# Optimization experiments

Hardware: AMD Instinct MI355X
Metric: run time of the kernel (lower is better)

Reference implementation:

```python
import jax, jax.numpy as jnp
import numpy as np

L, D, H, FF, V = 8, 768, 8, 2048, 32000
MAXLEN, TMAX = 512, 4
S = MAXLEN * TMAX  # 2048 context length
HD = D // H
EPS = 1e-4  # layer_norm_eps from module defaults


def setup_inputs() -> dict:
    key = jax.random.key(0)
    ks = jax.random.split(key, 16)
    s = 0.02
    B = 1
    rn = lambda k, shape: jax.random.normal(k, shape, jnp.float32) * s
    # sinusoidal positional encoding over MAXLEN real-token positions
    pos = np.arange(MAXLEN)[:, None]
    div = np.exp(np.arange(0, D, 2) * (-np.log(10000.0) / D))
    pe = np.zeros((MAXLEN, D), np.float32)
    pe[:, 0::2] = np.sin(pos * div)
    pe[:, 1::2] = np.cos(pos * div)
    return {
        "state_embeddings": jax.random.normal(ks[0], (B, S, D), jnp.float32),
        "padding_mask": jnp.zeros((B, S), bool),
        "pe": jnp.asarray(pe),
        "thought_emb": rn(ks[1], (TMAX, D)),
        "w_qkv": rn(ks[2], (L, 3 * D, D)),
        "b_qkv": jnp.zeros((L, 3 * D), jnp.float32),
        "w_out": rn(ks[3], (L, D, D)),
        "b_out": jnp.zeros((L, D), jnp.float32),
        "ln1_g": jnp.ones((L, D), jnp.float32),
        "ln1_b": jnp.zeros((L, D), jnp.float32),
        "ln2_g": jnp.ones((L, D), jnp.float32),
        "ln2_b": jnp.zeros((L, D), jnp.float32),
        "w_ff1": rn(ks[4], (L, FF, D)),
        "b_ff1": jnp.zeros((L, FF), jnp.float32),
        "w_ff2": rn(ks[5], (L, D, FF)),
        "b_ff2": jnp.zeros((L, D), jnp.float32),
        "fn_g": jnp.ones((D,), jnp.float32),
        "fn_b": jnp.zeros((D,), jnp.float32),
        "w_policy": rn(ks[6], (V, D)),
        "w_v1": rn(ks[7], (FF, D)),
        "b_v1": jnp.zeros((FF,), jnp.float32),
        "w_v2": rn(ks[8], (1, FF)),
        "b_v2": jnp.zeros((1,), jnp.float32),
        "n_thoughts_taken": 3,
    }


def _layer_norm(x, g, b):
    m = x.mean(-1, keepdims=True)
    v = ((x - m) ** 2).mean(-1, keepdims=True)
    return (x - m) / jnp.sqrt(v + EPS) * g + b


def reference(state_embeddings, padding_mask, pe, thought_emb, w_qkv, b_qkv, w_out, b_out, ln1_g, ln1_b, ln2_g, ln2_b, w_ff1, b_ff1, w_ff2, b_ff2, fn_g, fn_b, w_policy, w_v1, b_v1, w_v2, b_v2, n_thoughts_taken):
    tt = int(n_thoughts_taken)
    T = tt + 1  # block size (token + thoughts taken)
    B = state_embeddings.shape[0]
    R = MAXLEN  # real_token_count: all token slots real (no padding)
    # --- DualPositionalEncoding ---
    x = state_embeddings[:, :MAXLEN * T].reshape(B, MAXLEN, T, D)
    x = x + pe[None, :, None, :] + thought_emb[None, None, :T, :]
    x = x.reshape(B, MAXLEN * T, D)
    x = jnp.pad(x, ((0, 0), (0, S - MAXLEN * T), (0, 0)))
    # --- ThoughtsFormer block-causal mask (keep=True means attend) ---
    i = jnp.arange(S)
    tok, off = i // T, i % T
    same_block = (tok[:, None] == tok[None, :]) & (off[:, None] >= off[None, :]) & (tok[:, None] < R)
    global_cols = (off[None, :] == 0) & (tok[None, :] < R) & (i[:, None] > i[None, :]) & (i[:, None] < R * T)
    keep = (same_block | global_cols)[None, None] & (~padding_mask)[:, None, None, :]
    scale = 1.0 / np.sqrt(HD)

    def layer(h, p):
        wq, bq, wo, bo, g1, b1, g2, b2, wf1, bf1, wf2, bf2 = p
        # pre-norm self-attention
        y = _layer_norm(h, g1, b1)
        q, k, v = jnp.split(y @ wq.T + bq, 3, axis=-1)
        q = q.reshape(B, S, H, HD)
        k = k.reshape(B, S, H, HD)
        v = v.reshape(B, S, H, HD)
        scores = jnp.einsum('bihd,bjhd->bhij', q, k) * scale
        attn = jax.nn.softmax(jnp.where(keep, scores, -jnp.inf), axis=-1)
        o = jnp.einsum('bhij,bjhd->bihd', attn, v).reshape(B, S, D)
        h = h + o @ wo.T + bo
        # pre-norm FFN with exact (erf) GELU
        y = _layer_norm(h, g2, b2)
        h = h + jax.nn.gelu(y @ wf1.T + bf1, approximate=False) @ wf2.T + bf2
        h = jnp.where(jnp.isnan(h), 0.0, h)
        return h, None

    x, _ = jax.lax.scan(layer, x, (w_qkv, b_qkv, w_out, b_out, ln1_g, ln1_b, ln2_g, ln2_b, w_ff1, b_ff1, w_ff2, b_ff2))
    x = _layer_norm(x, fn_g, fn_b)  # TransformerEncoder final norm
    logits = x @ w_policy.T  # policy head (no bias)
    values = jax.nn.gelu(x @ w_v1.T + b_v1, approximate=False) @ w_v2.T + b_v2
    return logits, values
```

## Files before the change

### kernel.cpp

```cpp
#include <hip/hip_runtime.h>
#include <math.h>

#define S_TOT 2048
#define DMODEL 768
#define QKVD 2304
#define NHEAD 8
#define HDIM 96
#define FFDIM 2048
#define VOCAB 32000
#define MAXLEN_C 512
#define POL_CHUNK 3200
#define VLT_LD 2080
#define NEG_BIG (-3.0e38f)
#define M_INIT (-1.0e30f)
#define QK_SCALE 0.10206207261596575f

typedef __bf16 bf16x8 __attribute__((ext_vector_type(8)));
typedef float f32x4 __attribute__((ext_vector_type(4)));
typedef unsigned short u16x8 __attribute__((ext_vector_type(8)));
typedef unsigned short u16x4 __attribute__((ext_vector_type(4)));

__device__ __forceinline__ float gelu_exact(float x) {
  return 0.5f * x * (1.0f + erff(x * 0.70710678118654752f));
}

__device__ __forceinline__ float bf2f(unsigned short u) {
  union { unsigned int i; float f; } v;
  v.i = ((unsigned int)u) << 16;
  return v.f;
}

__device__ __forceinline__ unsigned short f2bf(float f) {
  union { float f; unsigned int i; } v;
  v.f = f;
  unsigned int x = v.i;
  return (unsigned short)((x + 0x7fffu + ((x >> 16) & 1u)) >> 16);
}

__device__ __forceinline__ unsigned int pack2bf(float a, float b) {
  return (unsigned int)f2bf(a) | ((unsigned int)f2bf(b) << 16);
}

__device__ __forceinline__ void gload_lds16(const unsigned short* g, unsigned short* l) {
  __builtin_amdgcn_global_load_lds(
      (const __attribute__((address_space(1))) unsigned int*)g,
      (__attribute__((address_space(3))) unsigned int*)l, 16, 0, 0);
}

__global__ __launch_bounds__(256) void embed_kernel(
    const float* __restrict__ se, const float* __restrict__ pe,
    const float* __restrict__ th, const int* __restrict__ ntt,
    float* __restrict__ X) {
  int idx = blockIdx.x * 256 + threadIdx.x;
  if (idx >= S_TOT * DMODEL) return;
  int p = idx / DMODEL;
  int d = idx - p * DMODEL;
  int T = ntt[0] + 1;
  float v = 0.0f;
  if (p < MAXLEN_C * T) {
    v = se[idx] + pe[(p / T) * DMODEL + d] + th[(p % T) * DMODEL + d];
  }
  X[idx] = v;
}

__global__ __launch_bounds__(256) void ln_bf_kernel(
    const float* __restrict__ X, const float* __restrict__ g,
    const float* __restrict__ b, unsigned short* __restrict__ Y) {
  __shared__ float red[4];
  const int row = blockIdx.x;
  const int tid = threadIdx.x;
  const float* x = X + (size_t)row * DMODEL;
  float v0 = x[tid], v1 = x[tid + 256], v2 = x[tid + 512];
  float s = v0 + v1 + v2;
  for (int o = 32; o; o >>= 1) s += __shfl_xor(s, o);
  if ((tid & 63) == 0) red[tid >> 6] = s;
  __syncthreads();
  float mean = (red[0] + red[1] + red[2] + red[3]) * (1.0f / DMODEL);
  float d0 = v0 - mean, d1 = v1 - mean, d2 = v2 - mean;
  float s2 = d0 * d0 + d1 * d1 + d2 * d2;
  for (int o = 32; o; o >>= 1) s2 += __shfl_xor(s2, o);
  __syncthreads();
  if ((tid & 63) == 0) red[tid >> 6] = s2;
  __syncthreads();
  float var = (red[0] + red[1] + red[2] + red[3]) * (1.0f / DMODEL);
  float rstd = rsqrtf(var + 1e-4f);
  unsigned short* y = Y + (size_t)row * DMODEL;
  y[tid]       = f2bf(d0 * rstd * g[tid]       + b[tid]);
  y[tid + 256] = f2bf(d1 * rstd * g[tid + 256] + b[tid + 256]);
  y[tid + 512] = f2bf(d2 * rstd * g[tid + 512] + b[tid + 512]);
}

__global__ __launch_bounds__(256) void cvt_kernel(
    const float* __restrict__ s, unsigned short* __restrict__ d, int n) {
  int i = (blockIdx.x * 256 + threadIdx.x) * 4;
  if (i >= n) return;
  float4 v = *(const float4*)(s + i);
  u16x4 o;
  o[0] = f2bf(v.x); o[1] = f2bf(v.y); o[2] = f2bf(v.z); o[3] = f2bf(v.w);
  *(u16x4*)(d + i) = o;
}

__global__ __launch_bounds__(256) void cvt4_kernel(
    const float* __restrict__ s0, const float* __restrict__ s1,
    const float* __restrict__ s2, const float* __restrict__ s3,
    unsigned short* __restrict__ d0, unsigned short* __restrict__ d1,
    unsigned short* __restrict__ d2, unsigned short* __restrict__ d3,
    int n0, int n1, int n2, int n3) {
  int i = (blockIdx.x * 256 + threadIdx.x) * 4;
  const float* s;
  unsigned short* d;
  if (i < n0) { s = s0; d = d0; }
  else if (i < n0 + n1) { i -= n0; s = s1; d = d1; }
  else if (i < n0 + n1 + n2) { i -= n0 + n1; s = s2; d = d2; }
  else if (i < n0 + n1 + n2 + n3) { i -= n0 + n1 + n2; s = s3; d = d3; }
  else return;
  float4 v = *(const float4*)(s + i);
  u16x4 o;
  o[0] = f2bf(v.x); o[1] = f2bf(v.y); o[2] = f2bf(v.z); o[3] = f2bf(v.w);
  *(u16x4*)(d + i) = o;
}

__global__ __launch_bounds__(256) void cvt6_kernel(
    const float* __restrict__ s0, const float* __restrict__ s1,
    const float* __restrict__ s2, const float* __restrict__ s3,
    const float* __restrict__ s4, const float* __restrict__ s5,
    unsigned short* __restrict__ d0, unsigned short* __restrict__ d1,
    unsigned short* __restrict__ d2, unsigned short* __restrict__ d3,
    unsigned short* __restrict__ d4, unsigned short* __restrict__ d5,
    int n0, int n1, int n2, int n3, int n4, int n5) {
  int i = (blockIdx.x * 256 + threadIdx.x) * 4;
  const float* s;
  unsigned short* d;
  if (i < n0) { s = s0; d = d0; }
  else if (i < n0 + n1) { i -= n0; s = s1; d = d1; }
  else if (i < n0 + n1 + n2) { i -= n0 + n1; s = s2; d = d2; }
  else if (i < n0 + n1 + n2 + n3) { i -= n0 + n1 + n2; s = s3; d = d3; }
  else if (i < n0 + n1 + n2 + n3 + n4) { i -= n0 + n1 + n2 + n3; s = s4; d = d4; }
  else if (i < n0 + n1 + n2 + n3 + n4 + n5) { i -= n0 + n1 + n2 + n3 + n4; s = s5; d = d5; }
  else return;
  float4 v = *(const float4*)(s + i);
  u16x4 o;
  o[0] = f2bf(v.x); o[1] = f2bf(v.y); o[2] = f2bf(v.z); o[3] = f2bf(v.w);
  *(u16x4*)(d + i) = o;
}

__global__ __launch_bounds__(256) void gemm_bf16_kernel(
    const unsigned short* __restrict__ A, const unsigned short* __restrict__ B,
    const float* __restrict__ bias, const float* __restrict__ res,
    void* __restrict__ Cout, int M, int N, int K, int ldc, int act, int outbf,
    int swiz) {
  __shared__ __align__(16) unsigned short As[3 * 4096];
  __shared__ __align__(16) unsigned short Bs[3 * 4096];
  const int t = threadIdx.x;
  const int w = t >> 6, l = t & 63;
  int n_blk, m_blk;
  if (swiz) {
    const int g = blockIdx.x;
    const int chunk = gridDim.x >> 3;
    const int logical = (g & 7) * chunk + (g >> 3);
    m_blk = logical & 15;
    n_blk = logical >> 4;
  } else {
    n_blk = blockIdx.x; m_blk = blockIdx.y;
  }
  const int n0 = n_blk * 128, i0 = m_blk * 128;
  const int wr = w >> 1, wc = w & 1;
  const int lr = l & 15;
  const int koff = (l >> 4) * 8;

  f32x4 acc[4][4] = {};

  const int srow = t >> 2;
  const int scol = (t & 3) * 8;
  const unsigned short* Ag = A + (size_t)(i0 + srow) * K + scol;
  const unsigned short* Bg = B + (size_t)(n0 + srow) * K + scol;
  const int lo0 = (w << 9);
  const int lo1 = 2048 + (w << 9);

#define STAGE128(buf, k0)                                        \
  do {                                                           \
    gload_lds16(Ag + (k0), &As[(buf) * 4096 + lo0]);             \
    gload_lds16(Ag + (size_t)64 * K + (k0), &As[(buf) * 4096 + lo1]); \
    gload_lds16(Bg + (k0), &Bs[(buf) * 4096 + lo0]);             \
    gload_lds16(Bg + (size_t)64 * K + (k0), &Bs[(buf) * 4096 + lo1]); \
  } while (0)

#define COMPUTE128(buf)                                                   \
  do {                                                                    \
    const unsigned short* Ab = &As[(buf) * 4096];                         \
    const unsigned short* Bb = &Bs[(buf) * 4096];                         \
    bf16x8 af[4], bfr[4];                                                 \
    _Pragma("unroll") for (int fi = 0; fi < 4; ++fi)                      \
        af[fi] = *(const bf16x8*)&Ab[(wr * 64 + fi * 16 + lr) * 32 + koff]; \
    _Pragma("unroll") for (int fj = 0; fj < 4; ++fj)                      \
        bfr[fj] = *(const bf16x8*)&Bb[(wc * 64 + fj * 16 + lr) * 32 + koff]; \
    _Pragma("unroll") for (int fi = 0; fi < 4; ++fi)                      \
      _Pragma("unroll") for (int fj = 0; fj < 4; ++fj)                    \
          acc[fi][fj] = __builtin_amdgcn_mfma_f32_16x16x32_bf16(          \
              bfr[fj], af[fi], acc[fi][fj], 0, 0, 0);                     \
  } while (0)

  const int nt = K >> 5;
  STAGE128(0, 0);
  if (nt > 1) STAGE128(1, 32);
  for (int tt = 0; tt < nt; ++tt) {
    const int cb = tt % 3;
    if (tt + 2 < nt) {
      STAGE128((tt + 2) % 3, (tt + 2) << 5);
      asm volatile("s_waitcnt vmcnt(8)" ::: "memory");
    } else if (tt + 1 < nt) {
      asm volatile("s_waitcnt vmcnt(4)" ::: "memory");
    } else {
      asm volatile("s_waitcnt vmcnt(0)" ::: "memory");
    }
    __builtin_amdgcn_s_barrier();
    __builtin_amdgcn_sched_barrier(0);
    COMPUTE128(cb);
    __builtin_amdgcn_sched_barrier(0);
    __builtin_amdgcn_s_barrier();
  }

  const int mloc = l & 15, ng = (l >> 4) * 4;
#pragma unroll
  for (int fi = 0; fi < 4; ++fi) {
    const int i = i0 + wr * 64 + fi * 16 + mloc;
    const size_t rowbase = (size_t)i * ldc;
#pragma unroll
    for (int fj = 0; fj < 4; ++fj) {
      const int nb = n0 + wc * 64 + fj * 16 + ng;
      float z0 = acc[fi][fj][0], z1 = acc[fi][fj][1];
      float z2 = acc[fi][fj][2], z3 = acc[fi][fj][3];
      if (bias) {
        float4 bv = *(const float4*)(bias + nb);
        z0 += bv.x; z1 += bv.y; z2 += bv.z; z3 += bv.w;
      }
      if (act) {
        z0 = gelu_exact(z0); z1 = gelu_exact(z1);
        z2 = gelu_exact(z2); z3 = gelu_exact(z3);
      }
      if (res) {
        float4 rv = *(const float4*)(res + rowbase + nb);
        z0 += rv.x; z1 += rv.y; z2 += rv.z; z3 += rv.w;
      }
      if (outbf) {
        u16x4 o;
        o[0] = f2bf(z0); o[1] = f2bf(z1); o[2] = f2bf(z2); o[3] = f2bf(z3);
        *(u16x4*)((unsigned short*)Cout + rowbase + nb) = o;
      } else {
        *(float4*)((float*)Cout + rowbase + nb) = make_float4(z0, z1, z2, z3);
      }
    }
  }
#undef STAGE128
#undef COMPUTE128
}

__global__ __launch_bounds__(256) void gemm64_bf16_kernel(
    const unsigned short* __restrict__ A, const unsigned short* __restrict__ B,
    const float* __restrict__ bias, const float* __restrict__ res,
    void* __restrict__ Cout, int M, int N, int K, int ldc, int act, int outbf) {
  __shared__ __align__(16) unsigned short As[3 * 4096];
  __shared__ __align__(16) unsigned short Bs[3 * 4096];
  const int t = threadIdx.x;
  const int w = t >> 6, l = t & 63;
  const int n0 = blockIdx.x * 64, i0 = blockIdx.y * 64;
  const int wr = w >> 1, wc = w & 1;
  const int lr = l & 15;
  const int koff = (l >> 4) * 8;

  f32x4 acc[2][2] = {};

  const int srow = t >> 2;
  const int scol = (t & 3) * 8;
  const unsigned short* Ag = A + (size_t)(i0 + srow) * K + scol;
  const unsigned short* Bg = B + (size_t)(n0 + srow) * K + scol;
  const int lo0 = (w << 9);
  const int lo1 = 2048 + (w << 9);

#define STAGE64(buf, k0)                                      \
  do {                                                        \
    gload_lds16(Ag + (k0), &As[(buf) * 4096 + lo0]);          \
    gload_lds16(Ag + (k0) + 32, &As[(buf) * 4096 + lo1]);     \
    gload_lds16(Bg + (k0), &Bs[(buf) * 4096 + lo0]);          \
    gload_lds16(Bg + (k0) + 32, &Bs[(buf) * 4096 + lo1]);     \
  } while (0)

#define COMPUTE64(buf)                                                        \
  do {                                                                        \
    const unsigned short* Ab = &As[(buf) * 4096];                             \
    const unsigned short* Bb = &Bs[(buf) * 4096];                             \
    bf16x8 af[2][2], bfr[2][2];                                               \
    _Pragma("unroll") for (int fi = 0; fi < 2; ++fi)                          \
      _Pragma("unroll") for (int kk = 0; kk < 2; ++kk)                        \
          af[fi][kk] = *(const bf16x8*)&Ab[kk * 2048 + (wr * 32 + fi * 16 + lr) * 32 + koff]; \
    _Pragma("unroll") for (int fj = 0; fj < 2; ++fj)                          \
      _Pragma("unroll") for (int kk = 0; kk < 2; ++kk)                        \
          bfr[fj][kk] = *(const bf16x8*)&Bb[kk * 2048 + (wc * 32 + fj * 16 + lr) * 32 + koff]; \
    _Pragma("unroll") for (int fi = 0; fi < 2; ++fi)                          \
      _Pragma("unroll") for (int fj = 0; fj < 2; ++fj)                        \
        _Pragma("unroll") for (int kk = 0; kk < 2; ++kk)                      \
            acc[fi][fj] = __builtin_amdgcn_mfma_f32_16x16x32_bf16(            \
                bfr[fj][kk], af[fi][kk], acc[fi][fj], 0, 0, 0);               \
  } while (0)

  const int nt = K >> 6;
  STAGE64(0, 0);
  if (nt > 1) STAGE64(1, 64);
  for (int tt = 0; tt < nt; ++tt) {
    const int cb = tt % 3;
    if (tt + 2 < nt) {
      STAGE64((tt + 2) % 3, (tt + 2) << 6);
      asm volatile("s_waitcnt vmcnt(8)" ::: "memory");
    } else if (tt + 1 < nt) {
      asm volatile("s_waitcnt vmcnt(4)" ::: "memory");
    } else {
      asm volatile("s_waitcnt vmcnt(0)" ::: "memory");
    }
    __builtin_amdgcn_s_barrier();
    __builtin_amdgcn_sched_barrier(0);
    COMPUTE64(cb);
    __builtin_amdgcn_sched_barrier(0);
    __builtin_amdgcn_s_barrier();
  }

  const int mloc = l & 15, ng = (l >> 4) * 4;
#pragma unroll
  for (int fi = 0; fi < 2; ++fi) {
    const int i = i0 + wr * 32 + fi * 16 + mloc;
    const size_t rowbase = (size_t)i * ldc;
#pragma unroll
    for (int fj = 0; fj < 2; ++fj) {
      const int nb = n0 + wc * 32 + fj * 16 + ng;
      float z0 = acc[fi][fj][0], z1 = acc[fi][fj][1];
      float z2 = acc[fi][fj][2], z3 = acc[fi][fj][3];
      if (bias) {
        float4 bv = *(const float4*)(bias + nb);
        z0 += bv.x; z1 += bv.y; z2 += bv.z; z3 += bv.w;
      }
      if (act) {
        z0 = gelu_exact(z0); z1 = gelu_exact(z1);
        z2 = gelu_exact(z2); z3 = gelu_exact(z3);
      }
      if (res) {
        float4 rv = *(const float4*)(res + rowbase + nb);
        z0 += rv.x; z1 += rv.y; z2 += rv.z; z3 += rv.w;
      }
      if (outbf) {
        u16x4 o;
        o[0] = f2bf(z0); o[1] = f2bf(z1); o[2] = f2bf(z2); o[3] = f2bf(z3);
        *(u16x4*)((unsigned short*)Cout + rowbase + nb) = o;
      } else {
        *(float4*)((float*)Cout + rowbase + nb) = make_float4(z0, z1, z2, z3);
      }
    }
  }
#undef STAGE64
#undef COMPUTE64
}

__global__ __launch_bounds__(256) void repack_kernel(
    const unsigned short* __restrict__ qkv, const int* __restrict__ ntt,
    unsigned short* __restrict__ Kg, unsigned short* __restrict__ Vgt,
    unsigned short* __restrict__ Vlt) {
  __shared__ unsigned short vt[64][104];
  const int pb = blockIdx.x * 64, h = blockIdx.y;
  const int T = ntt[0] + 1;
  const int tid = threadIdx.x;

  for (int idx = tid; idx < 64 * 96; idx += 256) {
    int pp = idx / 96, d = idx - pp * 96;
    vt[pp][d] = qkv[(size_t)(pb + pp) * QKVD + 2 * DMODEL + h * HDIM + d];
  }
  const int firstpp = (T - pb % T) % T;
  const int ng = (64 - firstpp + T - 1) / T;
  for (int idx = tid; idx < ng * 96; idx += 256) {
    int gi = idx / 96, d = idx - gi * 96;
    int p = pb + firstpp + gi * T;
    int g = p / T;
    if (g < MAXLEN_C)
      Kg[((size_t)h * 512 + g) * 96 + d] = qkv[(size_t)p * QKVD + DMODEL + h * HDIM + d];
  }
  __syncthreads();
  for (int idx = tid; idx < 96 * 64; idx += 256) {
    int d = idx >> 6, pp = idx & 63;
    Vlt[((size_t)h * 96 + d) * VLT_LD + pb + pp] = vt[pp][d];
  }
  for (int idx = tid; idx < ng * 96; idx += 256) {
    int d = idx / ng, gi = idx - d * ng;
    int pp = firstpp + gi * T;
    int g = (pb + pp) / T;
    if (g < MAXLEN_C && d < 96)
      Vgt[((size_t)h * 96 + d) * 512 + g] = vt[pp][d];
  }
}

__global__ __launch_bounds__(256) void attn_flash_kernel(
    const unsigned short* __restrict__ qkv, const unsigned short* __restrict__ Kg,
    const unsigned short* __restrict__ Vgt, const unsigned short* __restrict__ Vlt,
    const int* __restrict__ ntt, unsigned short* __restrict__ att) {
  __shared__ float Osh[4][96][17];
  __shared__ float Msh[4][16];
  __shared__ float Lsh[4][16];
  const int s = blockIdx.x, h = blockIdx.y;
  const int T = ntt[0] + 1;
  const int tid = threadIdx.x;
  const int w = tid >> 6, l = tid & 63;
  const int q15 = l & 15, grp = l >> 4;
  const int p0 = s * 16;
  const int p = p0 + q15;
  const int myTok = p / T;

  const unsigned short* qrow = qkv + (size_t)p * QKVD + h * HDIM + grp * 8;
  bf16x8 qf0 = *(const bf16x8*)(qrow);
  bf16x8 qf1 = *(const bf16x8*)(qrow + 32);
  bf16x8 qf2 = *(const bf16x8*)(qrow + 64);

  float m_run = M_INIT, l_run = 0.0f;
  f32x4 oacc[6] = {};

  const int gmax = (p0 + 15) / T;
  const int KP = (gmax >> 5) + 1;
  const unsigned short* KgH = Kg + (size_t)h * 512 * 96;
  const unsigned short* VgH = Vgt + (size_t)h * 96 * 512;

  for (int kp = w; kp < KP; kp += 4) {
    f32x4 s0 = {}, s1 = {};
    const unsigned short* k0r = KgH + (size_t)(kp * 32 + q15) * 96 + grp * 8;
    const unsigned short* k1r = k0r + 16 * 96;
    {
      bf16x8 a0 = *(const bf16x8*)(k0r);
      bf16x8 a1 = *(const bf16x8*)(k1r);
      bf16x8 b0 = *(const bf16x8*)(k0r + 32);
      bf16x8 b1 = *(const bf16x8*)(k1r + 32);
      bf16x8 c0 = *(const bf16x8*)(k0r + 64);
      bf16x8 c1 = *(const bf16x8*)(k1r + 64);
      __builtin_amdgcn_s_setprio(1);
      s0 = __builtin_amdgcn_mfma_f32_16x16x32_bf16(a0, qf0, s0, 0, 0, 0);
      s1 = __builtin_amdgcn_mfma_f32_16x16x32_bf16(a1, qf0, s1, 0, 0, 0);
      s0 = __builtin_amdgcn_mfma_f32_16x16x32_bf16(b0, qf1, s0, 0, 0, 0);
      s1 = __builtin_amdgcn_mfma_f32_16x16x32_bf16(b1, qf1, s1, 0, 0, 0);
      s0 = __builtin_amdgcn_mfma_f32_16x16x32_bf16(c0, qf2, s0, 0, 0, 0);
      s1 = __builtin_amdgcn_mfma_f32_16x16x32_bf16(c1, qf2, s1, 0, 0, 0);
      __builtin_amdgcn_s_setprio(0);
    }
    float sc[8];
#pragma unroll
    for (int e = 0; e < 4; ++e) {
      int g = kp * 32 + grp * 4 + e;
      sc[e] = (g * T <= p) ? s0[e] * QK_SCALE : NEG_BIG;
      g += 16;
      sc[4 + e] = (g * T <= p) ? s1[e] * QK_SCALE : NEG_BIG;
    }
    float tmax = sc[0];
#pragma unroll
    for (int e = 1; e < 8; ++e) tmax = fmaxf(tmax, sc[e]);
    tmax = fmaxf(tmax, __shfl_xor(tmax, 16));
    tmax = fmaxf(tmax, __shfl_xor(tmax, 32));
    float mnew = fmaxf(m_run, tmax);
    float alpha = __expf(m_run - mnew);
    float pv[8], ps = 0.0f;
#pragma unroll
    for (int e = 0; e < 8; ++e) { pv[e] = __expf(sc[e] - mnew); ps += pv[e]; }
    ps += __shfl_xor(ps, 16);
    ps += __shfl_xor(ps, 32);
    l_run = l_run * alpha + ps;
    m_run = mnew;
#pragma unroll
    for (int dt = 0; dt < 6; ++dt) oacc[dt] *= alpha;
    unsigned int pk0[2], pk1[2];
    pk0[0] = pack2bf(pv[0], pv[1]); pk0[1] = pack2bf(pv[2], pv[3]);
    pk1[0] = pack2bf(pv[4], pv[5]); pk1[1] = pack2bf(pv[6], pv[7]);
    union { unsigned int u[4]; bf16x8 v; } pf;
#pragma unroll
    for (int w2 = 0; w2 < 4; ++w2) {
      int src = (((grp & 1) << 1) + (w2 >> 1)) * 16 + q15;
      int y0 = __shfl((int)pk0[w2 & 1], src);
      int y1 = __shfl((int)pk1[w2 & 1], src);
      pf.u[w2] = (grp >> 1) ? (unsigned int)y1 : (unsigned int)y0;
    }
    __builtin_amdgcn_s_setprio(1);
#pragma unroll
    for (int dt = 0; dt < 6; ++dt) {
      bf16x8 vf = *(const bf16x8*)(VgH + (size_t)(dt * 16 + q15) * 512 + kp * 32 + grp * 8);
      oacc[dt] = __builtin_amdgcn_mfma_f32_16x16x32_bf16(vf, pf.v, oacc[dt], 0, 0, 0);
    }
    __builtin_amdgcn_s_setprio(0);
  }

  if (w == 3) {
    f32x4 s0 = {};
    const unsigned short* kl = qkv + (size_t)(p0 + q15) * QKVD + DMODEL + h * HDIM + grp * 8;
    __builtin_amdgcn_s_setprio(1);
    s0 = __builtin_amdgcn_mfma_f32_16x16x32_bf16(*(const bf16x8*)(kl), qf0, s0, 0, 0, 0);
    s0 = __builtin_amdgcn_mfma_f32_16x16x32_bf16(*(const bf16x8*)(kl + 32), qf1, s0, 0, 0, 0);
    s0 = __builtin_amdgcn_mfma_f32_16x16x32_bf16(*(const bf16x8*)(kl + 64), qf2, s0, 0, 0, 0);
    __builtin_amdgcn_s_setprio(0);
    float sc[4];
#pragma unroll
    for (int e = 0; e < 4; ++e) {
      int pk = p0 + grp * 4 + e;
      bool ok = (pk / T == myTok) && (pk % T != 0) && (pk <= p);
      sc[e] = ok ? s0[e] * QK_SCALE : NEG_BIG;
    }
    float tmax = fmaxf(fmaxf(sc[0], sc[1]), fmaxf(sc[2], sc[3]));
    tmax = fmaxf(tmax, __shfl_xor(tmax, 16));
    tmax = fmaxf(tmax, __shfl_xor(tmax, 32));
    float mnew = fmaxf(m_run, tmax);
    float alpha = __expf(m_run - mnew);
    float pv[4], ps = 0.0f;
#pragma unroll
    for (int e = 0; e < 4; ++e) { pv[e] = __expf(sc[e] - mnew); ps += pv[e]; }
    ps += __shfl_xor(ps, 16);
    ps += __shfl_xor(ps, 32);
    l_run = l_run * alpha + ps;
    m_run = mnew;
#pragma unroll
    for (int dt = 0; dt < 6; ++dt) oacc[dt] *= alpha;
    unsigned int pk0[2];
    pk0[0] = pack2bf(pv[0], pv[1]); pk0[1] = pack2bf(pv[2], pv[3]);
    union { unsigned int u[4]; bf16x8 v; } pf;
#pragma unroll
    for (int w2 = 0; w2 < 4; ++w2) {
      int src = (((grp & 1) << 1) + (w2 >> 1)) * 16 + q15;
      int y0 = __shfl((int)pk0[w2 & 1], src);
      pf.u[w2] = (grp >> 1) ? 0u : (unsigned int)y0;
    }
    __builtin_amdgcn_s_setprio(1);
#pragma unroll
    for (int dt = 0; dt < 6; ++dt) {
      bf16x8 vf = *(const bf16x8*)(Vlt + ((size_t)h * 96 + dt * 16 + q15) * VLT_LD + p0 + grp * 8);
      oacc[dt] = __builtin_amdgcn_mfma_f32_16x16x32_bf16(vf, pf.v, oacc[dt], 0, 0, 0);
    }
    __builtin_amdgcn_s_setprio(0);
  }

  if (l < 16) { Msh[w][l] = m_run; Lsh[w][l] = l_run; }
#pragma unroll
  for (int dt = 0; dt < 6; ++dt)
#pragma unroll
    for (int e = 0; e < 4; ++e)
      Osh[w][dt * 16 + grp * 4 + e][q15] = oacc[dt][e];
  __syncthreads();

  {
    const int q = tid & 15, dg = tid >> 4;
    float m0 = Msh[0][q], m1 = Msh[1][q], m2 = Msh[2][q], m3 = Msh[3][q];
    float ms = fmaxf(fmaxf(m0, m1), fmaxf(m2, m3));
    float c0 = __expf(m0 - ms), c1 = __expf(m1 - ms);
    float c2 = __expf(m2 - ms), c3 = __expf(m3 - ms);
    float lsum = c0 * Lsh[0][q] + c1 * Lsh[1][q] + c2 * Lsh[2][q] + c3 * Lsh[3][q];
    float rinv = 1.0f / lsum;
    unsigned short* orow = att + (size_t)(p0 + q) * DMODEL + h * HDIM;
#pragma unroll
    for (int j = 0; j < 6; ++j) {
      int d = dg * 6 + j;
      float o = c0 * Osh[0][d][q] + c1 * Osh[1][d][q] +
                c2 * Osh[2][d][q] + c3 * Osh[3][d][q];
      orow[d] = f2bf(o * rinv);
    }
  }
}

__global__ __launch_bounds__(256) void v2_kernel(
    const unsigned short* __restrict__ F1, const float* __restrict__ w2,
    const float* __restrict__ b2, float* __restrict__ out) {
  __shared__ float red[4];
  const int row = blockIdx.x;
  const int tid = threadIdx.x;
  float s = 0.0f;
  const unsigned short* xr = F1 + (size_t)row * FFDIM;
  for (int f = tid; f < FFDIM; f += 256) s += bf2f(xr[f]) * w2[f];
  for (int o = 32; o; o >>= 1) s += __shfl_xor(s, o);
  if ((tid & 63) == 0) red[tid >> 6] = s;
  __syncthreads();
  if (tid == 0) out[row] = red[0] + red[1] + red[2] + red[3] + b2[0];
}

extern "C" void kernel_launch(void* const* d_in, const int* in_sizes, int n_in,
                              void* d_out, int out_size, void* d_ws, size_t ws_size,
                              hipStream_t stream) {
  const float* se      = (const float*)d_in[0];
  const float* pe      = (const float*)d_in[2];
  const float* th      = (const float*)d_in[3];
  const float* w_qkv   = (const float*)d_in[4];
  const float* b_qkv   = (const float*)d_in[5];
  const float* w_out   = (const float*)d_in[6];
  const float* b_out   = (const float*)d_in[7];
  const float* ln1_g   = (const float*)d_in[8];
  const float* ln1_b   = (const float*)d_in[9];
  const float* ln2_g   = (const float*)d_in[10];
  const float* ln2_b   = (const float*)d_in[11];
  const float* w_ff1   = (const float*)d_in[12];
  const float* b_ff1   = (const float*)d_in[13];
  const float* w_ff2   = (const float*)d_in[14];
  const float* b_ff2   = (const float*)d_in[15];
  const float* fn_g    = (const float*)d_in[16];
  const float* fn_b    = (const float*)d_in[17];
  const float* w_pol   = (const float*)d_in[18];
  const float* w_v1    = (const float*)d_in[19];
  const float* b_v1    = (const float*)d_in[20];
  const float* w_v2    = (const float*)d_in[21];
  const float* b_v2    = (const float*)d_in[22];
  const int*   ntt     = (const int*)d_in[23];

  float* logits = (float*)d_out;
  float* values = logits + (size_t)S_TOT * VOCAB;

  const int nq = 3 * DMODEL * DMODEL, no = DMODEL * DMODEL;
  const int nf1 = FFDIM * DMODEL, nf2 = DMODEL * FFDIM;
  const int npol = VOCAB * DMODEL;

  char* p = (char*)d_ws;
  float* X             = (float*)p;          p += (size_t)S_TOT * DMODEL * 4;
  unsigned short* Ybf  = (unsigned short*)p; p += (size_t)S_TOT * DMODEL * 2;
  unsigned short* QKVb = (unsigned short*)p; p += (size_t)S_TOT * QKVD * 2;
  unsigned short* ATTb = (unsigned short*)p; p += (size_t)S_TOT * DMODEL * 2;
  unsigned short* F1b  = (unsigned short*)p; p += (size_t)S_TOT * FFDIM * 2;
  unsigned short* Kg   = (unsigned short*)p; p += (size_t)NHEAD * 512 * 96 * 2;
  unsigned short* Vgt  = (unsigned short*)p; p += (size_t)NHEAD * 96 * 512 * 2;
  unsigned short* Vlt  = (unsigned short*)p; p += (size_t)NHEAD * 96 * VLT_LD * 2;

  const size_t wbytes = ((size_t)8 * (nq + no + nf1 + nf2) + npol + nf1) * 2;
  const size_t used   = (size_t)(p - (char*)d_ws);
  const bool bigws = ws_size >= used + wbytes + (1u << 20);

  unsigned short *WqA, *WoA, *Wf1A, *Wf2A, *WpolA, *Wv1A;
  if (bigws) {
    WqA   = (unsigned short*)p; p += (size_t)8 * nq * 2;
    WoA   = (unsigned short*)p; p += (size_t)8 * no * 2;
    Wf1A  = (unsigned short*)p; p += (size_t)8 * nf1 * 2;
    Wf2A  = (unsigned short*)p; p += (size_t)8 * nf2 * 2;
    WpolA = (unsigned short*)p; p += (size_t)npol * 2;
    Wv1A  = (unsigned short*)p;
  } else {
    WqA   = (unsigned short*)p; p += (size_t)nq * 2;
    WoA   = (unsigned short*)p; p += (size_t)no * 2;
    Wf1A  = (unsigned short*)p; p += (size_t)nf1 * 2;
    Wf2A  = (unsigned short*)p; p += (size_t)nf2 * 2;
    WpolA = (unsigned short*)p;
    Wv1A  = Wf1A;
  }

  dim3 blk(256);

  if (bigws) {
    const int t0 = 8 * nq, t1 = 8 * no, t2 = 8 * nf1, t3 = 8 * nf2;
    const long total = (long)t0 + t1 + t2 + t3 + npol + nf1;
    cvt6_kernel<<<dim3((unsigned)((total / 4 + 255) / 256)), blk, 0, stream>>>(
        w_qkv, w_out, w_ff1, w_ff2, w_pol, w_v1,
        WqA, WoA, Wf1A, Wf2A, WpolA, Wv1A,
        t0, t1, t2, t3, npol, nf1);
  }

  embed_kernel<<<dim3((S_TOT * DMODEL + 255) / 256), blk, 0, stream>>>(se, pe, th, ntt, X);

  for (int l = 0; l < 8; ++l) {
    const unsigned short* pWq  = bigws ? WqA  + (size_t)l * nq  : WqA;
    const unsigned short* pWo  = bigws ? WoA  + (size_t)l * no  : WoA;
    const unsigned short* pWf1 = bigws ? Wf1A + (size_t)l * nf1 : Wf1A;
    const unsigned short* pWf2 = bigws ? Wf2A + (size_t)l * nf2 : Wf2A;
    if (!bigws) {
      const int ncvt4 = (nq + no + nf1 + nf2) / 4;
      cvt4_kernel<<<dim3((ncvt4 + 255) / 256), blk, 0, stream>>>(
          w_qkv + (size_t)l * nq, w_out + (size_t)l * no,
          w_ff1 + (size_t)l * nf1, w_ff2 + (size_t)l * nf2,
          WqA, WoA, Wf1A, Wf2A, nq, no, nf1, nf2);
    }

    ln_bf_kernel<<<dim3(S_TOT), blk, 0, stream>>>(X, ln1_g + l * DMODEL, ln1_b + l * DMODEL, Ybf);
    gemm64_bf16_kernel<<<dim3(QKVD / 64, S_TOT / 64), blk, 0, stream>>>(
        Ybf, pWq, b_qkv + (size_t)l * 3 * DMODEL, nullptr, QKVb,
        S_TOT, QKVD, DMODEL, QKVD, 0, 1);
    repack_kernel<<<dim3(S_TOT / 64, NHEAD), blk, 0, stream>>>(QKVb, ntt, Kg, Vgt, Vlt);
    attn_flash_kernel<<<dim3(S_TOT / 16, NHEAD), blk, 0, stream>>>(
        QKVb, Kg, Vgt, Vlt, ntt, ATTb);
    gemm64_bf16_kernel<<<dim3(DMODEL / 64, S_TOT / 64), blk, 0, stream>>>(
        ATTb, pWo, b_out + (size_t)l * DMODEL, X, X,
        S_TOT, DMODEL, DMODEL, DMODEL, 0, 0);

    ln_bf_kernel<<<dim3(S_TOT), blk, 0, stream>>>(X, ln2_g + l * DMODEL, ln2_b + l * DMODEL, Ybf);
    gemm64_bf16_kernel<<<dim3(FFDIM / 64, S_TOT / 64), blk, 0, stream>>>(
        Ybf, pWf1, b_ff1 + (size_t)l * FFDIM, nullptr, F1b,
        S_TOT, FFDIM, DMODEL, FFDIM, 1, 1);
    gemm64_bf16_kernel<<<dim3(DMODEL / 64, S_TOT / 64), blk, 0, stream>>>(
        F1b, pWf2, b_ff2 + (size_t)l * DMODEL, X, X,
        S_TOT, DMODEL, FFDIM, DMODEL, 0, 0);
  }

  ln_bf_kernel<<<dim3(S_TOT), blk, 0, stream>>>(X, fn_g, fn_b, Ybf);

  if (bigws) {
    gemm_bf16_kernel<<<dim3((S_TOT / 128) * (VOCAB / 128)), blk, 0, stream>>>(
        Ybf, WpolA, nullptr, nullptr, logits, S_TOT, VOCAB, DMODEL, VOCAB, 0, 0, 1);
  } else {
    for (int c = 0; c < VOCAB / POL_CHUNK; ++c) {
      cvt_kernel<<<dim3((POL_CHUNK * DMODEL / 4 + 255) / 256), blk, 0, stream>>>(
          w_pol + (size_t)c * POL_CHUNK * DMODEL, WpolA, POL_CHUNK * DMODEL);
      gemm_bf16_kernel<<<dim3(POL_CHUNK / 128, S_TOT / 128), blk, 0, stream>>>(
          Ybf, WpolA, nullptr, nullptr, logits + (size_t)c * POL_CHUNK,
          S_TOT, POL_CHUNK, DMODEL, VOCAB, 0, 0, 0);
    }
  }

  if (!bigws)
    cvt_kernel<<<dim3((nf1 / 4 + 255) / 256), blk, 0, stream>>>(w_v1, Wv1A, nf1);
  gemm64_bf16_kernel<<<dim3(FFDIM / 64, S_TOT / 64), blk, 0, stream>>>(
      Ybf, Wv1A, b_v1, nullptr, F1b, S_TOT, FFDIM, DMODEL, FFDIM, 1, 1);
  v2_kernel<<<dim3(S_TOT), blk, 0, stream>>>(F1b, w_v2, b_v2, values);
}
```

Baseline: 1.358 ms.

## Load A fragments directly from global into registers, stage only B in LDS

```diff
diff --git a/kernel.cpp b/kernel.cpp
--- a/kernel.cpp
+++ b/kernel.cpp
@@ -149,8 +149,7 @@
     const float* __restrict__ bias, const float* __restrict__ res,
     void* __restrict__ Cout, int M, int N, int K, int ldc, int act, int outbf,
     int swiz) {
-  __shared__ __align__(16) unsigned short As[3 * 4096];
-  __shared__ __align__(16) unsigned short Bs[3 * 4096];
+  __shared__ __align__(16) unsigned short Bs[2 * 4096];
   const int t = threadIdx.x;
   const int w = t >> 6, l = t & 63;
   int n_blk, m_blk;
@@ -172,50 +171,48 @@
 
   const int srow = t >> 2;
   const int scol = (t & 3) * 8;
-  const unsigned short* Ag = A + (size_t)(i0 + srow) * K + scol;
   const unsigned short* Bg = B + (size_t)(n0 + srow) * K + scol;
   const int lo0 = (w << 9);
   const int lo1 = 2048 + (w << 9);
-
-#define STAGE128(buf, k0)                                        \
+  const unsigned short* Abase = A + (size_t)(i0 + wr * 64 + lr) * K + koff;
+  const size_t Afs = (size_t)16 * K;
+
+#define STAGE_B(buf, k0)                                         \
   do {                                                           \
-    gload_lds16(Ag + (k0), &As[(buf) * 4096 + lo0]);             \
-    gload_lds16(Ag + (size_t)64 * K + (k0), &As[(buf) * 4096 + lo1]); \
     gload_lds16(Bg + (k0), &Bs[(buf) * 4096 + lo0]);             \
     gload_lds16(Bg + (size_t)64 * K + (k0), &Bs[(buf) * 4096 + lo1]); \
   } while (0)
 
-#define COMPUTE128(buf)                                                   \
-  do {                                                                    \
-    const unsigned short* Ab = &As[(buf) * 4096];                         \
-    const unsigned short* Bb = &Bs[(buf) * 4096];                         \
-    bf16x8 af[4], bfr[4];                                                 \
-    _Pragma("unroll") for (int fi = 0; fi < 4; ++fi)                      \
-        af[fi] = *(const bf16x8*)&Ab[(wr * 64 + fi * 16 + lr) * 32 + koff]; \
-    _Pragma("unroll") for (int fj = 0; fj < 4; ++fj)                      \
-        bfr[fj] = *(const bf16x8*)&Bb[(wc * 64 + fj * 16 + lr) * 32 + koff]; \
-    _Pragma("unroll") for (int fi = 0; fi < 4; ++fi)                      \
-      _Pragma("unroll") for (int fj = 0; fj < 4; ++fj)                    \
-          acc[fi][fj] = __builtin_amdgcn_mfma_f32_16x16x32_bf16(          \
-              bfr[fj], af[fi], acc[fi][fj], 0, 0, 0);                     \
-  } while (0)
-
   const int nt = K >> 5;
-  STAGE128(0, 0);
-  if (nt > 1) STAGE128(1, 32);
+  STAGE_B(0, 0);
   for (int tt = 0; tt < nt; ++tt) {
-    const int cb = tt % 3;
-    if (tt + 2 < nt) {
-      STAGE128((tt + 2) % 3, (tt + 2) << 5);
-      asm volatile("s_waitcnt vmcnt(8)" ::: "memory");
-    } else if (tt + 1 < nt) {
-      asm volatile("s_waitcnt vmcnt(4)" ::: "memory");
+    const int cb = tt & 1;
+    bf16x8 af0 = *(const bf16x8*)(Abase + 0 * Afs + (tt << 5));
+    bf16x8 af1 = *(const bf16x8*)(Abase + 1 * Afs + (tt << 5));
+    bf16x8 af2 = *(const bf16x8*)(Abase + 2 * Afs + (tt << 5));
+    bf16x8 af3 = *(const bf16x8*)(Abase + 3 * Afs + (tt << 5));
+    if (tt + 1 < nt) {
+      STAGE_B(cb ^ 1, (tt + 1) << 5);
+      asm volatile("s_waitcnt vmcnt(2)" ::: "memory");
     } else {
       asm volatile("s_waitcnt vmcnt(0)" ::: "memory");
     }
     __builtin_amdgcn_s_barrier();
     __builtin_amdgcn_sched_barrier(0);
-    COMPUTE128(cb);
+    {
+      const unsigned short* Bb = &Bs[cb * 4096];
+      bf16x8 bfr[4];
+#pragma unroll
+      for (int fj = 0; fj < 4; ++fj)
+        bfr[fj] = *(const bf16x8*)&Bb[(wc * 64 + fj * 16 + lr) * 32 + koff];
+#pragma unroll
+      for (int fj = 0; fj < 4; ++fj) {
+        acc[0][fj] = __builtin_amdgcn_mfma_f32_16x16x32_bf16(bfr[fj], af0, acc[0][fj], 0, 0, 0);
+        acc[1][fj] = __builtin_amdgcn_mfma_f32_16x16x32_bf16(bfr[fj], af1, acc[1][fj], 0, 0, 0);
+        acc[2][fj] = __builtin_amdgcn_mfma_f32_16x16x32_bf16(bfr[fj], af2, acc[2][fj], 0, 0, 0);
+        acc[3][fj] = __builtin_amdgcn_mfma_f32_16x16x32_bf16(bfr[fj], af3, acc[3][fj], 0, 0, 0);
+      }
+    }
     __builtin_amdgcn_sched_barrier(0);
     __builtin_amdgcn_s_barrier();
   }
@@ -251,16 +248,14 @@
       }
     }
   }
-#undef STAGE128
-#undef COMPUTE128
+#undef STAGE_B
 }
 
 __global__ __launch_bounds__(256) void gemm64_bf16_kernel(
     const unsigned short* __restrict__ A, const unsigned short* __restrict__ B,
     const float* __restrict__ bias, const float* __restrict__ res,
     void* __restrict__ Cout, int M, int N, int K, int ldc, int act, int outbf) {
-  __shared__ __align__(16) unsigned short As[3 * 4096];
-  __shared__ __align__(16) unsigned short Bs[3 * 4096];
+  __shared__ __align__(16) unsigned short Bs[2 * 4096];
   const int t = threadIdx.x;
   const int w = t >> 6, l = t & 63;
   const int n0 = blockIdx.x * 64, i0 = blockIdx.y * 64;
@@ -272,53 +267,50 @@
 
   const int srow = t >> 2;
   const int scol = (t & 3) * 8;
-  const unsigned short* Ag = A + (size_t)(i0 + srow) * K + scol;
   const unsigned short* Bg = B + (size_t)(n0 + srow) * K + scol;
   const int lo0 = (w << 9);
   const int lo1 = 2048 + (w << 9);
-
-#define STAGE64(buf, k0)                                      \
+  const unsigned short* Abase = A + (size_t)(i0 + wr * 32 + lr) * K + koff;
+  const size_t Afs = (size_t)16 * K;
+
+#define STAGE_B64(buf, k0)                                    \
   do {                                                        \
-    gload_lds16(Ag + (k0), &As[(buf) * 4096 + lo0]);          \
-    gload_lds16(Ag + (k0) + 32, &As[(buf) * 4096 + lo1]);     \
     gload_lds16(Bg + (k0), &Bs[(buf) * 4096 + lo0]);          \
     gload_lds16(Bg + (k0) + 32, &Bs[(buf) * 4096 + lo1]);     \
   } while (0)
 
-#define COMPUTE64(buf)                                                        \
-  do {                                                                        \
-    const unsigned short* Ab = &As[(buf) * 4096];                             \
-    const unsigned short* Bb = &Bs[(buf) * 4096];                             \
-    bf16x8 af[2][2], bfr[2][2];                                               \
-    _Pragma("unroll") for (int fi = 0; fi < 2; ++fi)                          \
-      _Pragma("unroll") for (int kk = 0; kk < 2; ++kk)                        \
-          af[fi][kk] = *(const bf16x8*)&Ab[kk * 2048 + (wr * 32 + fi * 16 + lr) * 32 + koff]; \
-    _Pragma("unroll") for (int fj = 0; fj < 2; ++fj)                          \
-      _Pragma("unroll") for (int kk = 0; kk < 2; ++kk)                        \
-          bfr[fj][kk] = *(const bf16x8*)&Bb[kk * 2048 + (wc * 32 + fj * 16 + lr) * 32 + koff]; \
-    _Pragma("unroll") for (int fi = 0; fi < 2; ++fi)                          \
-      _Pragma("unroll") for (int fj = 0; fj < 2; ++fj)                        \
-        _Pragma("unroll") for (int kk = 0; kk < 2; ++kk)                      \
-            acc[fi][fj] = __builtin_amdgcn_mfma_f32_16x16x32_bf16(            \
-                bfr[fj][kk], af[fi][kk], acc[fi][fj], 0, 0, 0);               \
-  } while (0)
-
   const int nt = K >> 6;
-  STAGE64(0, 0);
-  if (nt > 1) STAGE64(1, 64);
+  STAGE_B64(0, 0);
   for (int tt = 0; tt < nt; ++tt) {
-    const int cb = tt % 3;
-    if (tt + 2 < nt) {
-      STAGE64((tt + 2) % 3, (tt + 2) << 6);
-      asm volatile("s_waitcnt vmcnt(8)" ::: "memory");
-    } else if (tt + 1 < nt) {
-      asm volatile("s_waitcnt vmcnt(4)" ::: "memory");
+    const int cb = tt & 1;
+    const int k0 = tt << 6;
+    bf16x8 af00 = *(const bf16x8*)(Abase + 0 * Afs + k0);
+    bf16x8 af01 = *(const bf16x8*)(Abase + 0 * Afs + k0 + 32);
+    bf16x8 af10 = *(const bf16x8*)(Abase + 1 * Afs + k0);
+    bf16x8 af11 = *(const bf16x8*)(Abase + 1 * Afs + k0 + 32);
+    if (tt + 1 < nt) {
+      STAGE_B64(cb ^ 1, (tt + 1) << 6);
+      asm volatile("s_waitcnt vmcnt(2)" ::: "memory");
     } else {
       asm volatile("s_waitcnt vmcnt(0)" ::: "memory");
     }
     __builtin_amdgcn_s_barrier();
     __builtin_amdgcn_sched_barrier(0);
-    COMPUTE64(cb);
+    {
+      const unsigned short* Bb = &Bs[cb * 4096];
+      bf16x8 b00 = *(const bf16x8*)&Bb[(wc * 32 + 0 * 16 + lr) * 32 + koff];
+      bf16x8 b10 = *(const bf16x8*)&Bb[(wc * 32 + 1 * 16 + lr) * 32 + koff];
+      bf16x8 b01 = *(const bf16x8*)&Bb[2048 + (wc * 32 + 0 * 16 + lr) * 32 + koff];
+      bf16x8 b11 = *(const bf16x8*)&Bb[2048 + (wc * 32 + 1 * 16 + lr) * 32 + koff];
+      acc[0][0] = __builtin_amdgcn_mfma_f32_16x16x32_bf16(b00, af00, acc[0][0], 0, 0, 0);
+      acc[0][1] = __builtin_amdgcn_mfma_f32_16x16x32_bf16(b10, af00, acc[0][1], 0, 0, 0);
+      acc[1][0] = __builtin_amdgcn_mfma_f32_16x16x32_bf16(b00, af10, acc[1][0], 0, 0, 0);
+      acc[1][1] = __builtin_amdgcn_mfma_f32_16x16x32_bf16(b10, af10, acc[1][1], 0, 0, 0);
+      acc[0][0] = __builtin_amdgcn_mfma_f32_16x16x32_bf16(b01, af01, acc[0][0], 0, 0, 0);
+      acc[0][1] = __builtin_amdgcn_mfma_f32_16x16x32_bf16(b11, af01, acc[0][1], 0, 0, 0);
+      acc[1][0] = __builtin_amdgcn_mfma_f32_16x16x32_bf16(b01, af11, acc[1][0], 0, 0, 0);
+      acc[1][1] = __builtin_amdgcn_mfma_f32_16x16x32_bf16(b11, af11, acc[1][1], 0, 0, 0);
+    }
     __builtin_amdgcn_sched_barrier(0);
     __builtin_amdgcn_s_barrier();
   }
@@ -354,8 +346,7 @@
       }
     }
   }
-#undef STAGE64
-#undef COMPUTE64
+#undef STAGE_B64
 }
 
 __global__ __launch_bounds__(256) void repack_kernel(
```

Result: slower. 1.660 ms (+22.3%).
